# Performance work log

Measured on AMD Instinct MI355X. Metric: run time of the kernel, lower is better.

The kernel has to match this reference:

```python
import jax, jax.numpy as jnp
import numpy as np
import math

L = 2; B = 128; CIN = 64; E = 64; H = 8; Wd = 8; NH = 8; MEM = 40
HD = E // NH; HW = H * Wd; THD = HD * HW  # 512
MASK_B = 3.0; NEG = -1e9; EPS = 1e-5


def _conv(x, w, b):
    y = jax.lax.conv_general_dilated(x, w, (1, 1), 'SAME',
                                     dimension_numbers=('NCHW', 'OIHW', 'NCHW'))
    return y + b[None, :, None, None]


def setup_inputs() -> dict:
    key = jax.random.key(0)
    ks = jax.random.split(key, 12)
    f = jax.random.normal
    return {
        'x': f(ks[0], (B, CIN, H, Wd), jnp.float32),
        'h0': f(ks[1], (L, B, E, H, Wd), jnp.float32),
        'c0': f(ks[2], (L, B, E, H, Wd), jnp.float32),
        'k0': f(ks[3], (L, B, NH, MEM, THD), jnp.float32),
        'v0': f(ks[4], (L, B, NH, MEM, THD), jnp.float32),
        'src_mask': jax.random.randint(ks[5], (B, MEM), 0, 2).astype(bool),
        'notdone': jnp.ones((B,), bool),
        'main_w': f(ks[6], (L, 5 * E, CIN + 2 * E, 3, 3), jnp.float32) * 0.05,
        'main_b': jnp.zeros((L, 5 * E), jnp.float32),
        'proj_w': f(ks[7], (L, 3 * E, CIN + E, 3, 3), jnp.float32) * 0.05,
        'proj_b': jnp.zeros((L, 3 * E), jnp.float32),
        'out_w': f(ks[8], (L, E, E, 3, 3), jnp.float32) * 0.05,
        'out_b': jnp.zeros((L, E), jnp.float32),
        'ln_w': jnp.ones((L, E, H, Wd), jnp.float32),
        'ln_b': jnp.zeros((L, E, H, Wd), jnp.float32),
        'pos_w': f(ks[9], (L, MEM, HW * E), jnp.float32) * 0.05,
        'pos_b': f(ks[10], (L, MEM, NH), jnp.float32) * 0.05,
    }


def reference(x, h0, c0, k0, v0, src_mask, notdone,
              main_w, main_b, proj_w, proj_b, out_w, out_b,
              ln_w, ln_b, pos_w, pos_b):
    nd = notdone.astype(x.dtype)[:, None, None, None]
    # rolling attention mask: reset finished episodes, shift left, open last slot
    m = src_mask | (~notdone)[:, None]
    m = jnp.concatenate([m[:, 1:], jnp.zeros((B, 1), bool)], axis=1)
    bias = jnp.where(m, NEG, 0.0).astype(x.dtype)        # (B, MEM)
    bias = bias.at[:, -1].set(MASK_B)
    out = h0[L - 1] * nd
    for n in range(L):
        inp = jnp.concatenate([x, out], axis=1)          # (B, CIN+E, H, W)
        h_cur = h0[n] * nd
        c_cur = c0[n] * nd
        gates = _conv(jnp.concatenate([inp, h_cur], axis=1), main_w[n], main_b[n])
        cc_i, cc_f, cc_o, cc_g, cc_a = jnp.split(gates, 5, axis=1)
        i = jax.nn.sigmoid(cc_i)
        fg = jax.nn.sigmoid(cc_f)
        o = jax.nn.sigmoid(cc_o)
        g = jnp.tanh(cc_g)
        a = jax.nn.sigmoid(cc_a)
        c_next = fg * c_cur + i * g
        # attention over rolling memory (mem_n slots of flattened spatial features)
        kqv = _conv(inp, proj_w[n], proj_b[n]).reshape(B, NH, 3 * HD, HW)
        k = kqv[:, :, :HD].reshape(B, NH, THD)
        q = kqv[:, :, HD:2 * HD].reshape(B, NH, THD) / math.sqrt(THD)
        v = kqv[:, :, 2 * HD:].reshape(B, NH, THD)
        pw = pos_w[n].reshape(MEM, NH, THD).transpose(1, 0, 2)  # (NH, MEM, THD)
        k_cat = jnp.concatenate([k0[n][:, :, 1:], k[:, :, None, :]], axis=2) + pw[None]
        v_cat = jnp.concatenate([v0[n][:, :, 1:], v[:, :, None, :]], axis=2)
        scores = (jnp.einsum('bnd,bnmd->bnm', q, k_cat)
                  + bias[:, None, :] + pos_b[n].T[None])
        attn_w = jax.nn.softmax(scores, axis=-1)
        attn = jnp.einsum('bnm,bnmd->bnd', attn_w, v_cat).reshape(B, E, H, Wd)
        ao = _conv(attn, out_w[n], out_b[n]) + inp[:, :E]
        mu = ao.mean(axis=(1, 2, 3), keepdims=True)
        var = ((ao - mu) ** 2).mean(axis=(1, 2, 3), keepdims=True)
        ao = (ao - mu) * jax.lax.rsqrt(var + EPS) * ln_w[n][None] + ln_b[n][None]
        c_next = c_next + a * jnp.tanh(ao)
        out = o * jnp.tanh(c_next)
    return out
```

## Files before the change

### kernel.cpp

```cpp
#include <hip/hip_runtime.h>
#include <hip/hip_bf16.h>

typedef __hip_bfloat16 bf16;
typedef unsigned short u16;
typedef __attribute__((ext_vector_type(8))) short short8;
typedef __attribute__((ext_vector_type(4))) float f32x4;

#define Bb   128
#define MEMm 40

__device__ __forceinline__ float LD(const void* p, size_t i, int f32) {
    return f32 ? ((const float*)p)[i] : __bfloat162float(((const bf16*)p)[i]);
}
__device__ __forceinline__ float S2F(short s) {
    u16 u = (u16)s;
    return __bfloat162float(*(bf16*)&u);
}
__device__ __forceinline__ int LDB(const void* p, int i, int isbyte) {
    return isbyte ? (int)((const unsigned char*)p)[i] : ((const int*)p)[i];
}
__device__ __forceinline__ void SPLIT(float v, u16& hi, u16& lo) {
    bf16 h = __float2bfloat16(v);
    float r = v - __bfloat162float(h);
    bf16 l = __float2bfloat16(r);
    hi = *(u16*)&h; lo = *(u16*)&l;
}

__global__ void detect_kernel(const void* __restrict__ x,
                              const void* __restrict__ src_mask,
                              const void* __restrict__ notdone,
                              int* __restrict__ flags) {
    __shared__ int s[3];
    const int t = threadIdx.x;
    if (t < 3) s[t] = 0;
    __syncthreads();
    const bf16* xb = (const bf16*)x;
    int bad = 0;
    for (int i = t; i < 4096; i += 256) {
        float v = __bfloat162float(xb[2 * i]);
        if (!(fabsf(v) < 1e4f)) bad = 1;
    }
    if (bad) atomicOr(&s[0], 1);
    int mb = 0;
    const unsigned* mi = (const unsigned*)src_mask;
    for (int i = t; i < 1280; i += 256) if (mi[i] > 1u) mb = 1;
    if (mb) atomicOr(&s[1], 1);
    int nb = 0;
    const unsigned* ni = (const unsigned*)notdone;
    for (int i = t; i < 32; i += 256) if (ni[i] > 1u) nb = 1;
    if (nb) atomicOr(&s[2], 1);
    __syncthreads();
    if (t < 3) flags[t] = s[t];
}

__global__ void bias_kernel(const void* __restrict__ src_mask,
                            const void* __restrict__ notdone,
                            const int* __restrict__ flags,
                            float* __restrict__ biasb) {
    int idx = blockIdx.x * 256 + threadIdx.x;
    if (idx >= Bb * MEMm) return;
    const int mbyte = flags[1], ndbyte = flags[2];
    int b = idx / MEMm, m = idx - b * MEMm;
    float v;
    if (m == MEMm - 1) v = 3.0f;
    else {
        bool masked = (LDB(src_mask, b * MEMm + m + 1, mbyte) != 0) ||
                      (LDB(notdone, b, ndbyte) == 0);
        v = masked ? -1e9f : 0.f;
    }
    biasb[idx] = v;
}

__global__ void init_prevout_kernel(const void* __restrict__ h0,
                                    const void* __restrict__ notdone,
                                    const int* __restrict__ flags,
                                    float* __restrict__ outb, size_t off) {
    int idx = blockIdx.x * 256 + threadIdx.x;
    if (idx >= Bb * 512) return;
    const int isf32 = flags[0], ndbyte = flags[2];
    int b = idx >> 9;
    float nd = (LDB(notdone, b, ndbyte) != 0) ? 1.f : 0.f;
    size_t e = (size_t)idx * 8;
    float v[8];
    if (isf32) {
        const float* hp = (const float*)h0 + off + e;
        f32x4 a = *(const f32x4*)hp, c = *(const f32x4*)(hp + 4);
#pragma unroll
        for (int j = 0; j < 4; ++j) { v[j] = a[j]; v[4 + j] = c[j]; }
    } else {
        short8 s = *(const short8*)((const bf16*)h0 + off + e);
#pragma unroll
        for (int j = 0; j < 8; ++j) v[j] = S2F(s[j]);
    }
#pragma unroll
    for (int j = 0; j < 8; ++j) outb[e + j] = v[j] * nd;
}

__global__ void repack_w_kernel(const void* __restrict__ mw,
                                const void* __restrict__ pw,
                                const void* __restrict__ ow,
                                const int* __restrict__ flags,
                                u16* __restrict__ whi, u16* __restrict__ wlo) {
    int gi = blockIdx.x * 256 + threadIdx.x;
    if (gi >= 1622016) return;
    const int isf32 = flags[0];
    int layer = (gi >= 811008) ? 1 : 0;
    int i = gi - layer * 811008;
    float v;
    if (i < 552960) {
        int tap = i / 61440, r = i - tap * 61440, co = r / 192, ci = r - co * 192;
        v = LD(mw, (size_t)layer * 552960 + ((size_t)co * 192 + ci) * 9 + tap, isf32);
    } else if (i < 774144) {
        int j = i - 552960;
        int tap = j / 24576, r = j - tap * 24576, co = r / 128, ci = r - co * 128;
        v = LD(pw, (size_t)layer * 221184 + ((size_t)co * 128 + ci) * 9 + tap, isf32);
    } else {
        int j = i - 774144;
        int tap = j / 4096, r = j - tap * 4096, co = r / 64, ci = r - co * 64;
        v = LD(ow, (size_t)layer * 36864 + ((size_t)co * 64 + ci) * 9 + tap, isf32);
    }
    u16 h, l; SPLIT(v, h, l);
    whi[gi] = h; wlo[gi] = l;
}

__global__ __launch_bounds__(256) void build_cin_t_kernel(
    const void* __restrict__ x, const float* __restrict__ prev_out,
    const void* __restrict__ h0, const void* __restrict__ notdone,
    const int* __restrict__ flags,
    u16* __restrict__ cin_hi, u16* __restrict__ cin_lo, size_t hoff) {
    __shared__ float sb[192 * 65];
    const int t = threadIdx.x, b = blockIdx.x;
    const int isf32 = flags[0], ndbyte = flags[2];
    float nd = (LDB(notdone, b, ndbyte) != 0) ? 1.f : 0.f;
    for (int i = t; i < 12288; i += 256) {
        int c = i >> 6, px = i & 63;
        float v;
        if (c < 64)       v = LD(x, (size_t)b * 4096 + i, isf32);
        else if (c < 128) v = prev_out[(size_t)b * 4096 + i - 4096];
        else              v = LD(h0, hoff + (size_t)b * 4096 + i - 8192, isf32) * nd;
        sb[c * 65 + px] = v;
    }
    __syncthreads();
    size_t base = (size_t)b * 12288;
    for (int i = t; i < 12288; i += 256) {
        int px = i / 192, c = i - px * 192;
        float v = sb[c * 65 + px];
        u16 h, l; SPLIT(v, h, l);
        cin_hi[base + i] = h; cin_lo[base + i] = l;
    }
}

struct ConvArgs {
    const u16 *Ahi, *Alo;
    const u16 *WhiA, *WloA, *WhiB, *WloB;
    const void *biasA, *biasB;
    float *OutA, *OutB;
    long long boffA, boffB;
    int Astr, KciA, KciB, CoutA, CoutB, ntA, NT;
};

__global__ __launch_bounds__(256) void conv_mfma_kernel(ConvArgs g,
                                                        const int* __restrict__ flags) {
    __shared__ __align__(16) u16 Alds[4][2][2600];
    __shared__ __align__(16) u16 Wlds[2][2][2560];
    const int t = threadIdx.x, w = t >> 6, lane = t & 63;
    const int bx = blockIdx.x;
    const int nt = bx % g.NT, mblk = bx / g.NT;
    const bool isA = (nt < g.ntA);
    const u16* Whi = isA ? g.WhiA : g.WhiB;
    const u16* Wlo = isA ? g.WloA : g.WloB;
    const int Kci  = isA ? g.KciA : g.KciB;
    const int CoutT= isA ? g.CoutA : g.CoutB;
    float* Out     = isA ? g.OutA : g.OutB;
    const void* bias = isA ? g.biasA : g.biasB;
    const long long boff = isA ? g.boffA : g.boffB;
    const int n0 = (isA ? nt : nt - g.ntA) * 64;
    const int b = mblk * 4 + w;
    const int NITER = (Kci >> 5) * 9;
    const int isf32 = flags[0];

    if (lane < 40) { Alds[w][0][2560 + lane] = 0; Alds[w][1][2560 + lane] = 0; }

    f32x4 acc[4][4];
#pragma unroll
    for (int i = 0; i < 4; ++i)
#pragma unroll
        for (int j = 0; j < 4; ++j) { f32x4 z = {0.f, 0.f, 0.f, 0.f}; acc[i][j] = z; }

    const int co_l = t >> 2, jj = t & 3;
    uint4 hv, lv;
    auto issueW = [&](int it) {
        int kc = it / 9, tap = it - kc * 9;
        size_t o = ((size_t)(tap * CoutT + n0 + co_l)) * Kci + kc * 32 + jj * 8;
        hv = *(const uint4*)(Whi + o);
        lv = *(const uint4*)(Wlo + o);
    };

    issueW(0);
    for (int it = 0; it < NITER; ++it) {
        const int kc = it / 9, tap = it - kc * 9;
        const int par = it & 1;
        *(uint4*)&Wlds[par][0][co_l * 40 + jj * 8] = hv;
        *(uint4*)&Wlds[par][1][co_l * 40 + jj * 8] = lv;
        __syncthreads();
        if (it + 1 < NITER) issueW(it + 1);
        if (tap == 0) {
            size_t o = ((size_t)b * 64 + lane) * g.Astr + kc * 32;
            const uint4* sh = (const uint4*)(g.Ahi + o);
            const uint4* sl = (const uint4*)(g.Alo + o);
            uint4 a0 = sh[0], a1 = sh[1], a2 = sh[2], a3 = sh[3];
            uint4 c0 = sl[0], c1 = sl[1], c2 = sl[2], c3 = sl[3];
            *(uint4*)&Alds[w][0][lane * 40 + 0]  = a0;
            *(uint4*)&Alds[w][0][lane * 40 + 8]  = a1;
            *(uint4*)&Alds[w][0][lane * 40 + 16] = a2;
            *(uint4*)&Alds[w][0][lane * 40 + 24] = a3;
            *(uint4*)&Alds[w][1][lane * 40 + 0]  = c0;
            *(uint4*)&Alds[w][1][lane * 40 + 8]  = c1;
            *(uint4*)&Alds[w][1][lane * 40 + 16] = c2;
            *(uint4*)&Alds[w][1][lane * 40 + 24] = c3;
        }
        const int dy = tap / 3 - 1, dx = tap % 3 - 1;
        const int q8 = (lane >> 4) * 8;
        const int ml = lane & 15;
        short8 aH[4], aL[4];
#pragma unroll
        for (int mt = 0; mt < 4; ++mt) {
            int px = mt * 16 + ml;
            int yy = (px >> 3) + dy, xx = (px & 7) + dx;
            int row = ((unsigned)yy < 8u && (unsigned)xx < 8u) ? yy * 8 + xx : 64;
            int o = row * 40 + q8;
            aH[mt] = *(const short8*)&Alds[w][0][o];
            aL[mt] = *(const short8*)&Alds[w][1][o];
        }
#pragma unroll
        for (int nn = 0; nn < 4; ++nn) {
            int o = (nn * 16 + ml) * 40 + q8;
            short8 bH = *(const short8*)&Wlds[par][0][o];
            short8 bL = *(const short8*)&Wlds[par][1][o];
#pragma unroll
            for (int mt = 0; mt < 4; ++mt) {
                acc[mt][nn] = __builtin_amdgcn_mfma_f32_16x16x32_bf16(aH[mt], bH, acc[mt][nn], 0, 0, 0);
                acc[mt][nn] = __builtin_amdgcn_mfma_f32_16x16x32_bf16(aH[mt], bL, acc[mt][nn], 0, 0, 0);
                acc[mt][nn] = __builtin_amdgcn_mfma_f32_16x16x32_bf16(aL[mt], bH, acc[mt][nn], 0, 0, 0);
            }
        }
    }
    const int q = lane >> 4, ml = lane & 15;
#pragma unroll
    for (int nn = 0; nn < 4; ++nn) {
        int co = n0 + nn * 16 + ml;
        float bv = LD(bias, (size_t)boff + co, isf32);
#pragma unroll
        for (int mt = 0; mt < 4; ++mt) {
            f32x4 v = acc[mt][nn];
            v[0] += bv; v[1] += bv; v[2] += bv; v[3] += bv;
            *(f32x4*)&Out[((size_t)b * CoutT + co) * 64 + mt * 16 + q * 4] = v;
        }
    }
}

__global__ __launch_bounds__(256) void attn_kernel(
    const float* __restrict__ kqv,
    const void* __restrict__ k0,
    const void* __restrict__ v0,
    const void* __restrict__ pw,
    const void* __restrict__ pb,
    const float* __restrict__ biasb,
    const int* __restrict__ flags,
    u16* __restrict__ ahi, u16* __restrict__ alo,
    size_t kvoff, size_t pwoff, size_t pboff) {
    __shared__ float qv[512], kl[512], vl[512], sc[40], wexp[40];
    __shared__ float accbuf[4][512];
    const int t = threadIdx.x;
    const int isf32 = flags[0];
    const int b = blockIdx.x >> 3, h = blockIdx.x & 7;
    const size_t kqb = (size_t)b * 192 * 64;
    for (int d = t; d < 512; d += 256) {
        int hd = d >> 6, ss = d & 63;
        qv[d] = kqv[kqb + (h * 24 + 8 + hd) * 64 + ss] * 0.044194173824159216f;
        kl[d] = kqv[kqb + (h * 24 + 0 + hd) * 64 + ss];
        vl[d] = kqv[kqb + (h * 24 + 16 + hd) * 64 + ss];
    }
    __syncthreads();
    const int wid = t >> 6, lane = t & 63;
    const int d0 = lane * 8;
    const size_t kvbase = kvoff + ((size_t)(b * 8 + h)) * (size_t)(40 * 512);

    float q8[8];
#pragma unroll
    for (int j = 0; j < 8; ++j) q8[j] = qv[d0 + j];

    for (int m = wid; m < 40; m += 4) {
        float kc[8];
        if (m < 39) {
            if (isf32) {
                const float* kp = (const float*)k0 + kvbase + (size_t)(m + 1) * 512 + d0;
                f32x4 a = *(const f32x4*)kp, c = *(const f32x4*)(kp + 4);
#pragma unroll
                for (int j = 0; j < 4; ++j) { kc[j] = a[j]; kc[4 + j] = c[j]; }
            } else {
                short8 s = *(const short8*)((const bf16*)k0 + kvbase + (size_t)(m + 1) * 512 + d0);
#pragma unroll
                for (int j = 0; j < 8; ++j) kc[j] = S2F(s[j]);
            }
        } else {
#pragma unroll
            for (int j = 0; j < 8; ++j) kc[j] = kl[d0 + j];
        }
        if (isf32) {
            const float* pp = (const float*)pw + pwoff + (size_t)m * 4096 + h * 512 + d0;
            f32x4 a = *(const f32x4*)pp, c = *(const f32x4*)(pp + 4);
#pragma unroll
            for (int j = 0; j < 4; ++j) { kc[j] += a[j]; kc[4 + j] += c[j]; }
        } else {
            short8 s = *(const short8*)((const bf16*)pw + pwoff + (size_t)m * 4096 + h * 512 + d0);
#pragma unroll
            for (int j = 0; j < 8; ++j) kc[j] += S2F(s[j]);
        }
        float p = 0.f;
#pragma unroll
        for (int j = 0; j < 8; ++j) p += q8[j] * kc[j];
#pragma unroll
        for (int off = 32; off > 0; off >>= 1) p += __shfl_down(p, off, 64);
        if (lane == 0)
            sc[m] = p + biasb[b * 40 + m] + LD(pb, pboff + m * 8 + h, isf32);
    }
    __syncthreads();

    float mx = -1e30f;
    for (int m = 0; m < 40; ++m) mx = fmaxf(mx, sc[m]);
    if (t < 40) wexp[t] = __expf(sc[t] - mx);
    __syncthreads();
    float sum = 0.f;
    for (int m = 0; m < 40; ++m) sum += wexp[m];
    float rs = 1.f / sum;

    float acc8[8];
#pragma unroll
    for (int j = 0; j < 8; ++j) acc8[j] = 0.f;
    for (int m = wid; m < 40; m += 4) {
        float wgt = wexp[m];
        if (m < 39) {
            if (isf32) {
                const float* vp = (const float*)v0 + kvbase + (size_t)(m + 1) * 512 + d0;
                f32x4 a = *(const f32x4*)vp, c = *(const f32x4*)(vp + 4);
#pragma unroll
                for (int j = 0; j < 4; ++j) { acc8[j] += wgt * a[j]; acc8[4 + j] += wgt * c[j]; }
            } else {
                short8 s = *(const short8*)((const bf16*)v0 + kvbase + (size_t)(m + 1) * 512 + d0);
#pragma unroll
                for (int j = 0; j < 8; ++j) acc8[j] += wgt * S2F(s[j]);
            }
        } else {
#pragma unroll
            for (int j = 0; j < 8; ++j) acc8[j] += wgt * vl[d0 + j];
        }
    }
#pragma unroll
    for (int j = 0; j < 8; ++j) accbuf[wid][d0 + j] = acc8[j];
    __syncthreads();

    for (int d = t; d < 512; d += 256) {
        float acc = (accbuf[0][d] + accbuf[1][d]) + (accbuf[2][d] + accbuf[3][d]);
        acc *= rs;
        int ch = h * 8 + (d >> 6), px = d & 63;
        u16 hh, ll; SPLIT(acc, hh, ll);
        size_t o = (size_t)b * 4096 + px * 64 + ch;
        ahi[o] = hh; alo[o] = ll;
    }
}

__global__ __launch_bounds__(256) void ln_final_kernel(
    const float* __restrict__ convo,
    const void* __restrict__ x,
    const float* __restrict__ gates,
    const void* __restrict__ c0,
    const void* __restrict__ notdone,
    const void* __restrict__ lnw,
    const void* __restrict__ lnb,
    const int* __restrict__ flags,
    float* __restrict__ out_buf,
    void* __restrict__ dout, int write_out,
    size_t coff, size_t lnoff) {
    __shared__ float red[8];
    __shared__ float stats[2];
    const int t = threadIdx.x, b = blockIdx.x;
    const int isf32 = flags[0], ndbyte = flags[2];
    const size_t base = (size_t)b * 4096;
    float v[16];
    float sum = 0.f, sumsq = 0.f;
#pragma unroll
    for (int k = 0; k < 16; ++k) {
        int i = t + 256 * k;
        float val = convo[base + i] + LD(x, base + i, isf32);
        v[k] = val; sum += val; sumsq += val * val;
    }
#pragma unroll
    for (int off = 32; off > 0; off >>= 1) {
        sum   += __shfl_down(sum, off, 64);
        sumsq += __shfl_down(sumsq, off, 64);
    }
    const int wid = t >> 6, lane = t & 63;
    if (lane == 0) { red[wid] = sum; red[4 + wid] = sumsq; }
    __syncthreads();
    if (t == 0) {
        float ts = red[0] + red[1] + red[2] + red[3];
        float tq = red[4] + red[5] + red[6] + red[7];
        float mu = ts * (1.f / 4096.f);
        float var = tq * (1.f / 4096.f) - mu * mu;
        stats[0] = mu; stats[1] = rsqrtf(fmaxf(var, 0.f) + 1e-5f);
    }
    __syncthreads();
    float mu = stats[0], rstd = stats[1];
    float nd = (LDB(notdone, b, ndbyte) != 0) ? 1.f : 0.f;
    const size_t gbase = (size_t)b * 320 * 64;
#pragma unroll
    for (int k = 0; k < 16; ++k) {
        int i = t + 256 * k;
        int c = i >> 6, s = i & 63;
        float aon = (v[k] - mu) * rstd * LD(lnw, lnoff + i, isf32) + LD(lnb, lnoff + i, isf32);
        float gi = gates[gbase + (size_t)(c      ) * 64 + s];
        float gf = gates[gbase + (size_t)(c +  64) * 64 + s];
        float go = gates[gbase + (size_t)(c + 128) * 64 + s];
        float gg = gates[gbase + (size_t)(c + 192) * 64 + s];
        float ga = gates[gbase + (size_t)(c + 256) * 64 + s];
        gi = 1.f / (1.f + __expf(-gi));
        gf = 1.f / (1.f + __expf(-gf));
        go = 1.f / (1.f + __expf(-go));
        gg = tanhf(gg);
        ga = 1.f / (1.f + __expf(-ga));
        float cc = LD(c0, coff + base + i, isf32) * nd;
        float cn = gf * cc + gi * gg + ga * tanhf(aon);
        float o  = go * tanhf(cn);
        out_buf[base + i] = o;
        if (write_out) {
            if (isf32) ((float*)dout)[base + i] = o;
            else       ((bf16*)dout)[base + i] = __float2bfloat16(o);
        }
    }
}

extern "C" void kernel_launch(void* const* d_in, const int* in_sizes, int n_in,
                              void* d_out, int out_size, void* d_ws, size_t ws_size,
                              hipStream_t stream) {
    const void* x      = d_in[0];
    const void* h0     = d_in[1];
    const void* c0     = d_in[2];
    const void* k0     = d_in[3];
    const void* v0     = d_in[4];
    const void* src_mask = d_in[5];
    const void* notdone  = d_in[6];
    const void* main_w = d_in[7];
    const void* main_b = d_in[8];
    const void* proj_w = d_in[9];
    const void* proj_b = d_in[10];
    const void* out_w  = d_in[11];
    const void* out_b  = d_in[12];
    const void* ln_w   = d_in[13];
    const void* ln_b   = d_in[14];
    const void* pos_w  = d_in[15];
    const void* pos_b  = d_in[16];

    float* wsf = (float*)d_ws;
    int*   flags    = (int*)d_ws;
    float* bias_buf = wsf + 8;
    float* out_buf  = wsf + 8192;
    float* gates_buf= wsf + 532480;
    float* kqv_buf  = wsf + 3153920;
    u16* cin_hi     = (u16*)(wsf + 4726784);
    u16* cin_lo     = (u16*)(wsf + 5513216);
    float* convo_buf= wsf + 4726784;
    u16* attn_hi    = (u16*)(wsf + 5513216);
    u16* attn_lo    = (u16*)(wsf + 5775360);
    u16* wr_hi      = (u16*)(wsf + 6299648);
    u16* wr_lo      = (u16*)(wsf + 7110656);

    detect_kernel<<<1, 256, 0, stream>>>(x, src_mask, notdone, flags);
    bias_kernel<<<20, 256, 0, stream>>>(src_mask, notdone, flags, bias_buf);
    init_prevout_kernel<<<256, 256, 0, stream>>>(h0, notdone, flags, out_buf,
                                                 (size_t)524288);
    repack_w_kernel<<<6336, 256, 0, stream>>>(main_w, proj_w, out_w, flags,
                                              wr_hi, wr_lo);
    for (int n = 0; n < 2; ++n) {
        const size_t wb = (size_t)n * 811008;
        build_cin_t_kernel<<<128, 256, 0, stream>>>(x, out_buf, h0, notdone, flags,
                                                    cin_hi, cin_lo, (size_t)n * 524288);
        ConvArgs ga;
        ga.Ahi = cin_hi; ga.Alo = cin_lo; ga.Astr = 192;
        ga.WhiA = wr_hi + wb;          ga.WloA = wr_lo + wb;          ga.KciA = 192; ga.CoutA = 320;
        ga.WhiB = wr_hi + wb + 552960; ga.WloB = wr_lo + wb + 552960; ga.KciB = 128; ga.CoutB = 192;
        ga.biasA = main_b; ga.boffA = (long long)n * 320; ga.OutA = gates_buf;
        ga.biasB = proj_b; ga.boffB = (long long)n * 192; ga.OutB = kqv_buf;
        ga.ntA = 5; ga.NT = 8;
        conv_mfma_kernel<<<256, 256, 0, stream>>>(ga, flags);

        attn_kernel<<<1024, 256, 0, stream>>>(
            kqv_buf, k0, v0, pos_w, pos_b, bias_buf, flags, attn_hi, attn_lo,
            (size_t)n * 20971520, (size_t)n * 163840, (size_t)n * 320);

        ConvArgs oa;
        oa.Ahi = attn_hi; oa.Alo = attn_lo; oa.Astr = 64;
        oa.WhiA = wr_hi + wb + 774144; oa.WloA = wr_lo + wb + 774144; oa.KciA = 64; oa.CoutA = 64;
        oa.WhiB = oa.WhiA; oa.WloB = oa.WloA; oa.KciB = 64; oa.CoutB = 64;
        oa.biasA = out_b; oa.boffA = (long long)n * 64; oa.OutA = convo_buf;
        oa.biasB = out_b; oa.boffB = (long long)n * 64; oa.OutB = convo_buf;
        oa.ntA = 1; oa.NT = 1;
        conv_mfma_kernel<<<32, 256, 0, stream>>>(oa, flags);

        ln_final_kernel<<<128, 256, 0, stream>>>(
            convo_buf, x, gates_buf, c0, notdone, ln_w, ln_b, flags,
            out_buf, d_out, (n == 1) ? 1 : 0,
            (size_t)n * 524288, (size_t)n * 4096);
    }
}
```

Measured before the change: 640.6 us.

## Split conv work across wave pairs per batch and merge setup kernels

The MFMA conv kernel now assigns two waves to each batch element, with each wave computing half of the 64 output channels. This halves the per-wave accumulators and doubles the grid to 512 and 64 blocks, which should raise occupancy and the number of blocks in flight. A barrier is added after the A tile load into shared memory, since the two waves now load it cooperatively. Separately, the bias, initial previous-output and weight-repack kernels are merged into one launch to cut launch overhead.

```diff
diff --git a/kernel.cpp b/kernel.cpp
--- a/kernel.cpp
+++ b/kernel.cpp
@@ -53,74 +53,69 @@
     if (t < 3) flags[t] = s[t];
 }
 
-__global__ void bias_kernel(const void* __restrict__ src_mask,
-                            const void* __restrict__ notdone,
-                            const int* __restrict__ flags,
-                            float* __restrict__ biasb) {
-    int idx = blockIdx.x * 256 + threadIdx.x;
-    if (idx >= Bb * MEMm) return;
-    const int mbyte = flags[1], ndbyte = flags[2];
-    int b = idx / MEMm, m = idx - b * MEMm;
-    float v;
-    if (m == MEMm - 1) v = 3.0f;
-    else {
-        bool masked = (LDB(src_mask, b * MEMm + m + 1, mbyte) != 0) ||
-                      (LDB(notdone, b, ndbyte) == 0);
-        v = masked ? -1e9f : 0.f;
-    }
-    biasb[idx] = v;
-}
-
-__global__ void init_prevout_kernel(const void* __restrict__ h0,
-                                    const void* __restrict__ notdone,
-                                    const int* __restrict__ flags,
-                                    float* __restrict__ outb, size_t off) {
-    int idx = blockIdx.x * 256 + threadIdx.x;
-    if (idx >= Bb * 512) return;
-    const int isf32 = flags[0], ndbyte = flags[2];
-    int b = idx >> 9;
-    float nd = (LDB(notdone, b, ndbyte) != 0) ? 1.f : 0.f;
-    size_t e = (size_t)idx * 8;
-    float v[8];
-    if (isf32) {
-        const float* hp = (const float*)h0 + off + e;
-        f32x4 a = *(const f32x4*)hp, c = *(const f32x4*)(hp + 4);
-#pragma unroll
-        for (int j = 0; j < 4; ++j) { v[j] = a[j]; v[4 + j] = c[j]; }
+__global__ void setup_kernel(const void* __restrict__ src_mask,
+                             const void* __restrict__ notdone,
+                             const void* __restrict__ h0,
+                             const void* __restrict__ mw,
+                             const void* __restrict__ pw,
+                             const void* __restrict__ ow,
+                             const int* __restrict__ flags,
+                             float* __restrict__ biasb,
+                             float* __restrict__ outb, size_t hoff,
+                             u16* __restrict__ whi, u16* __restrict__ wlo) {
+    const int bid = blockIdx.x, t = threadIdx.x;
+    const int isf32 = flags[0], mbyte = flags[1], ndbyte = flags[2];
+    if (bid < 20) {
+        int idx = bid * 256 + t;
+        if (idx >= Bb * MEMm) return;
+        int b = idx / MEMm, m = idx - b * MEMm;
+        float v;
+        if (m == MEMm - 1) v = 3.0f;
+        else {
+            bool masked = (LDB(src_mask, b * MEMm + m + 1, mbyte) != 0) ||
+                          (LDB(notdone, b, ndbyte) == 0);
+            v = masked ? -1e9f : 0.f;
+        }
+        biasb[idx] = v;
+    } else if (bid < 276) {
+        int idx = (bid - 20) * 256 + t;
+        int b = idx >> 9;
+        float nd = (LDB(notdone, b, ndbyte) != 0) ? 1.f : 0.f;
+        size_t e = (size_t)idx * 8;
+        float v[8];
+        if (isf32) {
+            const float* hp = (const float*)h0 + hoff + e;
+            f32x4 a = *(const f32x4*)hp, c = *(const f32x4*)(hp + 4);
+#pragma unroll
+            for (int j = 0; j < 4; ++j) { v[j] = a[j]; v[4 + j] = c[j]; }
+        } else {
+            short8 s = *(const short8*)((const bf16*)h0 + hoff + e);
+#pragma unroll
+            for (int j = 0; j < 8; ++j) v[j] = S2F(s[j]);
+        }
+#pragma unroll
+        for (int j = 0; j < 8; ++j) outb[e + j] = v[j] * nd;
     } else {
-        short8 s = *(const short8*)((const bf16*)h0 + off + e);
-#pragma unroll
-        for (int j = 0; j < 8; ++j) v[j] = S2F(s[j]);
-    }
-#pragma unroll
-    for (int j = 0; j < 8; ++j) outb[e + j] = v[j] * nd;
-}
-
-__global__ void repack_w_kernel(const void* __restrict__ mw,
-                                const void* __restrict__ pw,
-                                const void* __restrict__ ow,
-                                const int* __restrict__ flags,
-                                u16* __restrict__ whi, u16* __restrict__ wlo) {
-    int gi = blockIdx.x * 256 + threadIdx.x;
-    if (gi >= 1622016) return;
-    const int isf32 = flags[0];
-    int layer = (gi >= 811008) ? 1 : 0;
-    int i = gi - layer * 811008;
-    float v;
-    if (i < 552960) {
-        int tap = i / 61440, r = i - tap * 61440, co = r / 192, ci = r - co * 192;
-        v = LD(mw, (size_t)layer * 552960 + ((size_t)co * 192 + ci) * 9 + tap, isf32);
-    } else if (i < 774144) {
-        int j = i - 552960;
-        int tap = j / 24576, r = j - tap * 24576, co = r / 128, ci = r - co * 128;
-        v = LD(pw, (size_t)layer * 221184 + ((size_t)co * 128 + ci) * 9 + tap, isf32);
-    } else {
-        int j = i - 774144;
-        int tap = j / 4096, r = j - tap * 4096, co = r / 64, ci = r - co * 64;
-        v = LD(ow, (size_t)layer * 36864 + ((size_t)co * 64 + ci) * 9 + tap, isf32);
-    }
-    u16 h, l; SPLIT(v, h, l);
-    whi[gi] = h; wlo[gi] = l;
+        int gi = (bid - 276) * 256 + t;
+        if (gi >= 1622016) return;
+        int layer = (gi >= 811008) ? 1 : 0;
+        int i = gi - layer * 811008;
+        float v;
+        if (i < 552960) {
+            int tap = i / 61440, r = i - tap * 61440, co = r / 192, ci = r - co * 192;
+            v = LD(mw, (size_t)layer * 552960 + ((size_t)co * 192 + ci) * 9 + tap, isf32);
+        } else if (i < 774144) {
+            int j = i - 552960;
+            int tap = j / 24576, r = j - tap * 24576, co = r / 128, ci = r - co * 128;
+            v = LD(pw, (size_t)layer * 221184 + ((size_t)co * 128 + ci) * 9 + tap, isf32);
+        } else {
+            int j = i - 774144;
+            int tap = j / 4096, r = j - tap * 4096, co = r / 64, ci = r - co * 64;
+            v = LD(ow, (size_t)layer * 36864 + ((size_t)co * 64 + ci) * 9 + tap, isf32);
+        }
+        u16 h, l; SPLIT(v, h, l);
+        whi[gi] = h; wlo[gi] = l;
+    }
 }
 
 __global__ __launch_bounds__(256) void build_cin_t_kernel(
@@ -161,9 +156,10 @@
 
 __global__ __launch_bounds__(256) void conv_mfma_kernel(ConvArgs g,
                                                         const int* __restrict__ flags) {
-    __shared__ __align__(16) u16 Alds[4][2][2600];
+    __shared__ __align__(16) u16 Alds[2][2][2600];
     __shared__ __align__(16) u16 Wlds[2][2][2560];
     const int t = threadIdx.x, w = t >> 6, lane = t & 63;
+    const int bpair = w >> 1, half = w & 1;
     const int bx = blockIdx.x;
     const int nt = bx % g.NT, mblk = bx / g.NT;
     const bool isA = (nt < g.ntA);
@@ -175,17 +171,17 @@
     const void* bias = isA ? g.biasA : g.biasB;
     const long long boff = isA ? g.boffA : g.boffB;
     const int n0 = (isA ? nt : nt - g.ntA) * 64;
-    const int b = mblk * 4 + w;
+    const int b = mblk * 2 + bpair;
     const int NITER = (Kci >> 5) * 9;
     const int isf32 = flags[0];
 
-    if (lane < 40) { Alds[w][0][2560 + lane] = 0; Alds[w][1][2560 + lane] = 0; }
-
-    f32x4 acc[4][4];
+    if (half == 0 && lane < 40) { Alds[bpair][0][2560 + lane] = 0; Alds[bpair][1][2560 + lane] = 0; }
+
+    f32x4 acc[4][2];
 #pragma unroll
     for (int i = 0; i < 4; ++i)
 #pragma unroll
-        for (int j = 0; j < 4; ++j) { f32x4 z = {0.f, 0.f, 0.f, 0.f}; acc[i][j] = z; }
+        for (int j = 0; j < 2; ++j) { f32x4 z = {0.f, 0.f, 0.f, 0.f}; acc[i][j] = z; }
 
     const int co_l = t >> 2, jj = t & 3;
     uint4 hv, lv;
@@ -205,19 +201,18 @@
         __syncthreads();
         if (it + 1 < NITER) issueW(it + 1);
         if (tap == 0) {
-            size_t o = ((size_t)b * 64 + lane) * g.Astr + kc * 32;
+            int arow = half * 32 + (lane >> 1);
+            int chalf = (lane & 1) * 16;
+            size_t o = ((size_t)b * 64 + arow) * g.Astr + kc * 32 + chalf;
             const uint4* sh = (const uint4*)(g.Ahi + o);
             const uint4* sl = (const uint4*)(g.Alo + o);
-            uint4 a0 = sh[0], a1 = sh[1], a2 = sh[2], a3 = sh[3];
-            uint4 c0 = sl[0], c1 = sl[1], c2 = sl[2], c3 = sl[3];
-            *(uint4*)&Alds[w][0][lane * 40 + 0]  = a0;
-            *(uint4*)&Alds[w][0][lane * 40 + 8]  = a1;
-            *(uint4*)&Alds[w][0][lane * 40 + 16] = a2;
-            *(uint4*)&Alds[w][0][lane * 40 + 24] = a3;
-            *(uint4*)&Alds[w][1][lane * 40 + 0]  = c0;
-            *(uint4*)&Alds[w][1][lane * 40 + 8]  = c1;
-            *(uint4*)&Alds[w][1][lane * 40 + 16] = c2;
-            *(uint4*)&Alds[w][1][lane * 40 + 24] = c3;
+            uint4 a0 = sh[0], a1 = sh[1];
+            uint4 c0 = sl[0], c1 = sl[1];
+            *(uint4*)&Alds[bpair][0][arow * 40 + chalf + 0] = a0;
+            *(uint4*)&Alds[bpair][0][arow * 40 + chalf + 8] = a1;
+            *(uint4*)&Alds[bpair][1][arow * 40 + chalf + 0] = c0;
+            *(uint4*)&Alds[bpair][1][arow * 40 + chalf + 8] = c1;
+            __syncthreads();
         }
         const int dy = tap / 3 - 1, dx = tap % 3 - 1;
         const int q8 = (lane >> 4) * 8;
@@ -229,12 +224,12 @@
             int yy = (px >> 3) + dy, xx = (px & 7) + dx;
             int row = ((unsigned)yy < 8u && (unsigned)xx < 8u) ? yy * 8 + xx : 64;
             int o = row * 40 + q8;
-            aH[mt] = *(const short8*)&Alds[w][0][o];
-            aL[mt] = *(const short8*)&Alds[w][1][o];
-        }
-#pragma unroll
-        for (int nn = 0; nn < 4; ++nn) {
-            int o = (nn * 16 + ml) * 40 + q8;
+            aH[mt] = *(const short8*)&Alds[bpair][0][o];
+            aL[mt] = *(const short8*)&Alds[bpair][1][o];
+        }
+#pragma unroll
+        for (int nn = 0; nn < 2; ++nn) {
+            int o = (half * 32 + nn * 16 + ml) * 40 + q8;
             short8 bH = *(const short8*)&Wlds[par][0][o];
             short8 bL = *(const short8*)&Wlds[par][1][o];
 #pragma unroll
@@ -247,8 +242,8 @@
     }
     const int q = lane >> 4, ml = lane & 15;
 #pragma unroll
-    for (int nn = 0; nn < 4; ++nn) {
-        int co = n0 + nn * 16 + ml;
+    for (int nn = 0; nn < 2; ++nn) {
+        int co = n0 + half * 32 + nn * 16 + ml;
         float bv = LD(bias, (size_t)boff + co, isf32);
 #pragma unroll
         for (int mt = 0; mt < 4; ++mt) {
@@ -476,11 +471,10 @@
     u16* wr_lo      = (u16*)(wsf + 7110656);
 
     detect_kernel<<<1, 256, 0, stream>>>(x, src_mask, notdone, flags);
-    bias_kernel<<<20, 256, 0, stream>>>(src_mask, notdone, flags, bias_buf);
-    init_prevout_kernel<<<256, 256, 0, stream>>>(h0, notdone, flags, out_buf,
-                                                 (size_t)524288);
-    repack_w_kernel<<<6336, 256, 0, stream>>>(main_w, proj_w, out_w, flags,
-                                              wr_hi, wr_lo);
+    setup_kernel<<<6612, 256, 0, stream>>>(src_mask, notdone, h0,
+                                           main_w, proj_w, out_w, flags,
+                                           bias_buf, out_buf, (size_t)524288,
+                                           wr_hi, wr_lo);
     for (int n = 0; n < 2; ++n) {
         const size_t wb = (size_t)n * 811008;
         build_cin_t_kernel<<<128, 256, 0, stream>>>(x, out_buf, h0, notdone, flags,
@@ -492,7 +486,7 @@
         ga.biasA = main_b; ga.boffA = (long long)n * 320; ga.OutA = gates_buf;
         ga.biasB = proj_b; ga.boffB = (long long)n * 192; ga.OutB = kqv_buf;
         ga.ntA = 5; ga.NT = 8;
-        conv_mfma_kernel<<<256, 256, 0, stream>>>(ga, flags);
+        conv_mfma_kernel<<<512, 256, 0, stream>>>(ga, flags);
 
         attn_kernel<<<1024, 256, 0, stream>>>(
             kqv_buf, k0, v0, pos_w, pos_b, bias_buf, flags, attn_hi, attn_lo,
@@ -505,7 +499,7 @@
         oa.biasA = out_b; oa.boffA = (long long)n * 64; oa.OutA = convo_buf;
         oa.biasB = out_b; oa.boffB = (long long)n * 64; oa.OutB = convo_buf;
         oa.ntA = 1; oa.NT = 1;
-        conv_mfma_kernel<<<32, 256, 0, stream>>>(oa, flags);
+        conv_mfma_kernel<<<64, 256, 0, stream>>>(oa, flags);
 
         ln_final_kernel<<<128, 256, 0, stream>>>(
             convo_buf, x, gates_buf, c0, notdone, ln_w, ln_b, flags,
```

Result: faster. 614.2 us (-4.1%).
